# Kernel optimization log

Hardware: AMD Instinct MI355X
Metric: run time of the kernel (lower is better)

Reference implementation:

```python
import jax, jax.numpy as jnp
import numpy as np
import math

B, A, C = 16, 8732, 91
K = 400            # backend.topk_candidates (per-class top-k before NMS)
D = 200            # backend.detections_per_img
TOPK = 2           # extractor topk_candidates (classes returned per box)
SCORE_THRESH = 0.01
NMS_THRESH = 0.45
IMG = 300.0        # SSD300 image size (boxes clipped to [0, IMG])
BBOX_XFORM_CLIP = math.log(1000.0 / 16.0)


def setup_inputs() -> dict:
    key = jax.random.key(0)
    k1, k2, k3, k4 = jax.random.split(key, 4)
    cls_logits = jax.random.normal(k1, (B, A, C), jnp.float32)
    bbox_regression = jax.random.normal(k2, (B, A, 4), jnp.float32) * 0.5
    # valid anchors in xyxy with positive width/height
    cxcy = jax.random.uniform(k3, (A, 2), jnp.float32, 0.0, IMG)
    wh = jax.random.uniform(k4, (A, 2), jnp.float32, 8.0, 96.0)
    anchors = jnp.concatenate([cxcy - 0.5 * wh, cxcy + 0.5 * wh], axis=-1)
    return {"cls_logits": cls_logits, "bbox_regression": bbox_regression, "anchors": anchors}


def _decode(rel, anchors):
    # torchvision BoxCoder.decode_single, weights (10, 10, 5, 5)
    wa = anchors[:, 2] - anchors[:, 0]
    ha = anchors[:, 3] - anchors[:, 1]
    cxa = anchors[:, 0] + 0.5 * wa
    cya = anchors[:, 1] + 0.5 * ha
    dx = rel[:, 0] / 10.0
    dy = rel[:, 1] / 10.0
    dw = jnp.minimum(rel[:, 2] / 5.0, BBOX_XFORM_CLIP)
    dh = jnp.minimum(rel[:, 3] / 5.0, BBOX_XFORM_CLIP)
    cx = dx * wa + cxa
    cy = dy * ha + cya
    w = jnp.exp(dw) * wa
    h = jnp.exp(dh) * ha
    boxes = jnp.stack([cx - 0.5 * w, cy - 0.5 * h, cx + 0.5 * w, cy + 0.5 * h], axis=-1)
    return jnp.clip(boxes, 0.0, IMG)  # clip_boxes_to_image


def _iou_one_vs_all(box, boxes):
    x1 = jnp.maximum(box[0], boxes[:, 0])
    y1 = jnp.maximum(box[1], boxes[:, 1])
    x2 = jnp.minimum(box[2], boxes[:, 2])
    y2 = jnp.minimum(box[3], boxes[:, 3])
    inter = jnp.clip(x2 - x1, 0.0) * jnp.clip(y2 - y1, 0.0)
    a1 = (box[2] - box[0]) * (box[3] - box[1])
    a2 = (boxes[:, 2] - boxes[:, 0]) * (boxes[:, 3] - boxes[:, 1])
    return inter / (a1 + a2 - inter + 1e-9)


def _image_forward(logits, rel, anchors):
    probs = jax.nn.softmax(logits, axis=-1)          # [A, C]
    boxes = _decode(rel, anchors)                    # [A, 4]
    # per-class threshold + top-k (labels 1..C-1), padded fixed-size version
    fg = probs[:, 1:]                                # [A, C-1]
    masked = jnp.where(fg > SCORE_THRESH, fg, -1.0)
    vals, idxs = jax.lax.top_k(masked.T, K)          # [C-1, K]
    cand_boxes = boxes[idxs]                         # [C-1, K, 4]
    cand_all = probs[idxs]                           # [C-1, K, C]
    labels = jnp.broadcast_to(jnp.arange(1, C, dtype=jnp.int32)[:, None], (C - 1, K))
    valid = vals > SCORE_THRESH
    N = (C - 1) * K
    fb = cand_boxes.reshape(N, 4)
    fs = vals.reshape(N)
    fl = labels.reshape(N)
    fa = cand_all.reshape(N, C)
    fv = valid.reshape(N)
    # batched_nms: offset boxes per class so different classes never overlap
    off = fl.astype(jnp.float32) * (IMG + 2.0)
    ob = fb + off[:, None]
    s0 = jnp.where(fv, fs, -jnp.inf)

    def body(i, carry):
        s, keep, kscore = carry
        j = jnp.argmax(s)
        keep = keep.at[i].set(j.astype(jnp.int32))
        kscore = kscore.at[i].set(s[j])
        iou = _iou_one_vs_all(ob[j], ob)
        s = jnp.where(iou > NMS_THRESH, -jnp.inf, s)
        return s, keep, kscore

    _, keep, kscore = jax.lax.fori_loop(
        0, D, body,
        (s0, jnp.zeros(D, jnp.int32), jnp.full((D,), -jnp.inf, jnp.float32)))
    kvalid = kscore > -jnp.inf                       # padding rows (fewer than D dets)
    out_boxes = jnp.where(kvalid[:, None], fb[keep], 0.0)          # [D, 4]
    top_scores, tidx = jax.lax.top_k(fa[keep][:, 1:], TOPK)        # [D, TOPK]
    top_scores = jnp.where(kvalid[:, None], top_scores, 0.0)
    out_labels = jnp.where(kvalid[:, None], tidx + 1, 0)
    return out_boxes, top_scores, out_labels


def reference(cls_logits, bbox_regression, anchors):
    return jax.vmap(_image_forward, in_axes=(0, 0, None))(cls_logits, bbox_regression, anchors)
```

## Files before the change

### kernel.cpp

```cpp
#include <hip/hip_runtime.h>
#include <cstdint>
#include <cstddef>

#define B_N   16
#define A_N   8732
#define C_N   91
#define FG_N  90
#define K_TOP 400
#define D_N   200
#define NTASK (B_N * FG_N)
#define K1_APB 128
#define K1_NBLK ((A_N + K1_APB - 1) / K1_APB)
#define K4_T  1024
#define NBIN  2048

__global__ __launch_bounds__(128) void k1_softmax_decode(
    const float* __restrict__ cls, const float* __restrict__ reg,
    const float* __restrict__ anc, float* __restrict__ probs_t,
    float* __restrict__ boxes)
{
#pragma clang fp contract(off)
  __shared__ float4 lds4[(K1_APB * C_N + 3) / 4];
  float* lds = (float*)lds4;
  const int bb = blockIdx.x;
  const int b = bb / K1_NBLK;
  const int blk = bb - b * K1_NBLK;
  const int a0 = blk * K1_APB;
  const int nloc = (A_N - a0) < K1_APB ? (A_N - a0) : K1_APB;
  const int tid = threadIdx.x;

  const size_t gbase_f4 = ((size_t)(b * A_N + a0) * C_N) >> 2;
  const size_t TOT_F4 = ((size_t)B_N * A_N * C_N) >> 2;
  const float4* cls4 = (const float4*)cls;
  constexpr int NF4 = (K1_APB * C_N) / 4;
  for (int i = tid; i < NF4; i += K1_APB) {
    size_t g = gbase_f4 + i;
    if (g < TOT_F4) lds4[i] = cls4[g];
  }
  __syncthreads();

  if (tid >= nloc) return;
  const int a = a0 + tid;
  const int tg = b * A_N + a;
  float* lg = lds + tid * C_N;

  float m = lg[0];
  for (int c = 1; c < C_N; ++c) m = fmaxf(m, lg[c]);
  float s = 0.0f;
  for (int c = 0; c < C_N; ++c) {
    float e = expf(lg[c] - m);
    s += e;
    lg[c] = e;
  }
  for (int c = 1; c < C_N; ++c)
    probs_t[((size_t)b * FG_N + (c - 1)) * A_N + a] = lg[c] / s;

  float4 rl = *(const float4*)(reg + (size_t)tg * 4);
  float4 an = *(const float4*)(anc + (size_t)a * 4);
  float wa = an.z - an.x;
  float ha = an.w - an.y;
  float cxa = an.x + 0.5f * wa;
  float cya = an.y + 0.5f * ha;
  float dx = rl.x / 10.0f;
  float dy = rl.y / 10.0f;
  const float clipv = 4.135166556742356f;
  float dw = fminf(rl.z / 5.0f, clipv);
  float dh = fminf(rl.w / 5.0f, clipv);
  float t1 = dx * wa;  float cx = t1 + cxa;
  float t2 = dy * ha;  float cy = t2 + cya;
  float w = expf(dw) * wa;
  float h = expf(dh) * ha;
  float4 out;
  out.x = fminf(fmaxf(cx - 0.5f * w, 0.0f), 300.0f);
  out.y = fminf(fmaxf(cy - 0.5f * h, 0.0f), 300.0f);
  out.z = fminf(fmaxf(cx + 0.5f * w, 0.0f), 300.0f);
  out.w = fminf(fmaxf(cy + 0.5f * h, 0.0f), 300.0f);
  *(float4*)(boxes + (size_t)tg * 4) = out;
}

__device__ __forceinline__ void scan_select(int* hist, int nbins, int need,
                                            int tid, int* chunk, int* res)
{
  int per = nbins >> 8;
  if (tid < 256) {
    int s = 0;
    for (int i = 0; i < per; ++i) s += hist[tid * per + i];
    chunk[tid] = s;
  }
  __syncthreads();
  if (tid == 0) {
    int cum = 0;
    for (int t2 = 255; t2 >= 0; --t2) { int v = chunk[t2]; chunk[t2] = cum; cum += v; }
  }
  __syncthreads();
  if (tid < 256) {
    int cum = chunk[tid];
    for (int i = per - 1; i >= 0; --i) {
      int bn = tid * per + i;
      int h = hist[bn];
      if (cum < need && need <= cum + h) { res[0] = bn; res[1] = cum; }
      cum += h;
    }
  }
  __syncthreads();
}

__device__ __forceinline__ void desc_scan256(int* chunk, int* s_total, int tid)
{
  if (tid < 64) {
    const int l = tid;
    int e0 = chunk[4 * l + 0];
    int e1 = chunk[4 * l + 1];
    int e2 = chunk[4 * l + 2];
    int e3 = chunk[4 * l + 3];
    int ls = e0 + e1 + e2 + e3;
    int suf = ls;
#pragma unroll
    for (int d = 1; d < 64; d <<= 1) {
      int o = __shfl(suf, l + d, 64);
      if (l + d < 64) suf += o;
    }
    int excl = suf - ls;
    chunk[4 * l + 3] = excl;
    chunk[4 * l + 2] = excl + e3;
    chunk[4 * l + 1] = excl + e3 + e2;
    chunk[4 * l + 0] = excl + e3 + e2 + e1;
    if (l == 0) *s_total = suf;
  }
}

__global__ __launch_bounds__(256) void k23_topk_nms(
    const float* __restrict__ probs_t, const float* __restrict__ boxes,
    int* __restrict__ topk_anchor,
    unsigned long long* __restrict__ kept_key, int* __restrict__ kept_cnt)
{
#pragma clang fp contract(off)
  __shared__ __align__(16) int cnt[NBIN];
  __shared__ unsigned long long sorted[1024];
  __shared__ int chunk[256];
  __shared__ int res[2];
  __shared__ int s_total;
  __shared__ int s_bad;
  __shared__ int s_lcnt;
  __shared__ unsigned long long s_supm[4];
  __shared__ int s_nk;
  const int task = blockIdx.x;
  const int tid = threadIdx.x;
  const float* sc = probs_t + (size_t)task * A_N;
  const float4* sc4 = (const float4*)sc;
  constexpr int NV4 = A_N >> 2;

  for (int i = tid; i < NBIN; i += 256) cnt[i] = 0;
  if (tid == 0) s_bad = 0;
  __syncthreads();

  for (int i = tid; i < NV4; i += 256) {
    float4 p4 = sc4[i];
    if (p4.x > 0.01f) atomicAdd(&cnt[(__float_as_uint(p4.x) >> 15) & 0x7FFu], 1);
    if (p4.y > 0.01f) atomicAdd(&cnt[(__float_as_uint(p4.y) >> 15) & 0x7FFu], 1);
    if (p4.z > 0.01f) atomicAdd(&cnt[(__float_as_uint(p4.z) >> 15) & 0x7FFu], 1);
    if (p4.w > 0.01f) atomicAdd(&cnt[(__float_as_uint(p4.w) >> 15) & 0x7FFu], 1);
  }
  __syncthreads();
  {
    int s = 0;
    for (int i = 0; i < 8; ++i) s += cnt[tid * 8 + i];
    chunk[tid] = s;
  }
  __syncthreads();
  desc_scan256(chunk, &s_total, tid);
  __syncthreads();
  {
    int acc = chunk[tid];
    for (int i = 7; i >= 0; --i) {
      int bn = tid * 8 + i;
      int h = cnt[bn];
      cnt[bn] = acc;
      acc += h;
    }
  }
  __syncthreads();
  const int total = s_total;
  const int ksel = total < K_TOP ? total : K_TOP;

  for (int i = tid; i < NV4; i += 256) {
    float4 p4 = sc4[i];
    const unsigned a0 = (unsigned)(i * 4);
    if (p4.x > 0.01f) {
      unsigned k = __float_as_uint(p4.x);
      int pos = atomicAdd(&cnt[(k >> 15) & 0x7FFu], 1);
      if (pos < 1024)
        sorted[pos] = ((unsigned long long)k << 32) | (0xFFFFFFFFu - a0);
    }
    if (p4.y > 0.01f) {
      unsigned k = __float_as_uint(p4.y);
      int pos = atomicAdd(&cnt[(k >> 15) & 0x7FFu], 1);
      if (pos < 1024)
        sorted[pos] = ((unsigned long long)k << 32) | (0xFFFFFFFFu - (a0 + 1));
    }
    if (p4.z > 0.01f) {
      unsigned k = __float_as_uint(p4.z);
      int pos = atomicAdd(&cnt[(k >> 15) & 0x7FFu], 1);
      if (pos < 1024)
        sorted[pos] = ((unsigned long long)k << 32) | (0xFFFFFFFFu - (a0 + 2));
    }
    if (p4.w > 0.01f) {
      unsigned k = __float_as_uint(p4.w);
      int pos = atomicAdd(&cnt[(k >> 15) & 0x7FFu], 1);
      if (pos < 1024)
        sorted[pos] = ((unsigned long long)k << 32) | (0xFFFFFFFFu - (a0 + 3));
    }
  }
  __syncthreads();
  for (int i = 0; i < 8; ++i) {
    int bn = tid * 8 + i;
    int end0 = cnt[bn];
    int start = (bn < NBIN - 1) ? cnt[bn + 1] : 0;
    int cb = end0 - start;
    if (cb > 1 && start < K_TOP) {
      if (end0 > 1024) { s_bad = 1; continue; }
      for (int q = start + 1; q < end0; ++q) {
        unsigned long long v = sorted[q];
        int j = q - 1;
        while (j >= start && sorted[j] < v) { sorted[j + 1] = sorted[j]; --j; }
        sorted[j + 1] = v;
      }
    }
  }
  __syncthreads();

  if (s_bad) {
    for (int i = tid; i < NBIN; i += 256) cnt[i] = 0;
    __syncthreads();
    for (int a = tid; a < A_N; a += 256) {
      float p = sc[a];
      if (p > 0.01f) atomicAdd(&cnt[__float_as_uint(p) >> 21], 1);
    }
    __syncthreads();
    int need = K_TOP;
    scan_select(cnt, 2048, need, tid, chunk, res);
    const unsigned b1 = (unsigned)res[0];
    const int above1 = res[1];
    const int in1 = cnt[b1];
    __syncthreads();
    unsigned cutoff;
    if (above1 + in1 <= 1024) {
      cutoff = b1 << 21;
    } else {
      need -= above1;
      for (int i = tid; i < NBIN; i += 256) cnt[i] = 0;
      __syncthreads();
      for (int a = tid; a < A_N; a += 256) {
        float p = sc[a];
        if (p > 0.01f) {
          unsigned k = __float_as_uint(p);
          if ((k >> 21) == b1) atomicAdd(&cnt[(k >> 10) & 0x7FFu], 1);
        }
      }
      __syncthreads();
      scan_select(cnt, 2048, need, tid, chunk, res);
      const unsigned b2 = (unsigned)res[0];
      need -= res[1];
      const unsigned pre22 = (b1 << 11) | b2;
      __syncthreads();
      for (int i = tid; i < 1024; i += 256) cnt[i] = 0;
      __syncthreads();
      for (int a = tid; a < A_N; a += 256) {
        float p = sc[a];
        if (p > 0.01f) {
          unsigned k = __float_as_uint(p);
          if ((k >> 10) == pre22) atomicAdd(&cnt[k & 0x3FFu], 1);
        }
      }
      __syncthreads();
      scan_select(cnt, 1024, need, tid, chunk, res);
      cutoff = (pre22 << 10) | (unsigned)res[0];
      __syncthreads();
    }
    if (tid == 0) s_lcnt = 0;
    __syncthreads();
    for (int a = tid; a < A_N; a += 256) {
      float p = sc[a];
      if (p > 0.01f) {
        unsigned k = __float_as_uint(p);
        if (k >= cutoff) {
          int pos = atomicAdd(&s_lcnt, 1);
          if (pos < 1024)
            sorted[pos] = ((unsigned long long)k << 32) | (unsigned)(0xFFFFFFFFu - (unsigned)a);
        }
      }
    }
    __syncthreads();
    const int n = s_lcnt < 1024 ? s_lcnt : 1024;
    const int W = (n <= 512) ? 512 : 1024;
    for (int i = tid; i < W; i += 256) if (i >= n) sorted[i] = 0ULL;
    __syncthreads();
    for (int kk = 2; kk <= W; kk <<= 1) {
      for (int jj = kk >> 1; jj > 0; jj >>= 1) {
        for (int i = tid; i < W; i += 256) {
          int ix = i ^ jj;
          if (ix > i) {
            unsigned long long va = sorted[i], vb = sorted[ix];
            bool desc = ((i & kk) == 0);
            if (desc ? (va < vb) : (va > vb)) { sorted[i] = vb; sorted[ix] = va; }
          }
        }
        __syncthreads();
      }
    }
  }

  for (int r = tid; r < ksel; r += 256) {
    unsigned long long v = sorted[r];
    topk_anchor[(size_t)task * K_TOP + r] =
        (int)(0xFFFFFFFFu - (unsigned)(v & 0xFFFFFFFFull));
  }
  if (tid == 0) s_nk = 0;
  __syncthreads();

  float4* keptb  = (float4*)cnt;
  float*  kepta  = (float*)(cnt + 800);
  int*    keptr  = cnt + 1000;
  float4* chunkb = (float4*)(cnt + 1200);
  unsigned long long* colpart =
      (unsigned long long*)(cnt + 1456);

  const int wid  = tid >> 6;
  const int lane = tid & 63;
  const int b = task / FG_N;
  const int c = task - b * FG_N;
  const float off = (float)(c + 1) * 302.0f;
  const float* bx = boxes + (size_t)b * (A_N * 4);

  float4 nxt = make_float4(0.0f, 0.0f, 0.0f, 0.0f);
  if (lane < ksel) {
    int a0 = (int)(0xFFFFFFFFu - (unsigned)(sorted[lane] & 0xFFFFFFFFull));
    nxt = *(const float4*)(bx + (size_t)a0 * 4);
  }
  for (int c0 = 0; c0 < ksel; c0 += 64) {
    float4 cur = nxt;
    int nidx = c0 + 64 + lane;
    if (nidx < ksel) {
      int an = (int)(0xFFFFFFFFu - (unsigned)(sorted[nidx] & 0xFFFFFFFFull));
      nxt = *(const float4*)(bx + (size_t)an * 4);
    }
    const int rem = ksel - c0;
    cur.x += off; cur.y += off; cur.z += off; cur.w += off;
    const float area = (cur.z - cur.x) * (cur.w - cur.y);
    const int nk = s_nk;

    chunkb[lane] = cur;
    unsigned long long part = 0ULL;
    {
      const int jn = rem < 64 ? rem : 64;
      const int j0 = wid << 4;
      const int j1 = (j0 + 16) < jn ? (j0 + 16) : jn;
      for (int j = j0; j < j1; ++j) {
        float4 bj = chunkb[j];
        float ja = (bj.z - bj.x) * (bj.w - bj.y);
        float ix1 = fmaxf(bj.x, cur.x);
        float iy1 = fmaxf(bj.y, cur.y);
        float ix2 = fminf(bj.z, cur.z);
        float iy2 = fminf(bj.w, cur.w);
        float inter = fmaxf(ix2 - ix1, 0.0f) * fmaxf(iy2 - iy1, 0.0f);
        float denom = ja + area - inter + 1e-9f;
        float thr = 0.45f * denom;
        bool s_sup = inter > thr;
        bool amb = fabsf(inter - thr) <= 1.5e-6f * thr;
        if (amb) s_sup = (inter / denom) > 0.45f;
        if (s_sup && j != lane) part |= 1ULL << j;
      }
    }
    colpart[(wid << 6) | lane] = part;

    bool sup = false;
    for (int k = wid; k < nk; k += 4) {
      if (__all(sup)) break;
      float4 kb = keptb[k];
      float  ka = kepta[k];
      float ix1 = fmaxf(cur.x, kb.x);
      float iy1 = fmaxf(cur.y, kb.y);
      float ix2 = fminf(cur.z, kb.z);
      float iy2 = fminf(cur.w, kb.w);
      float inter = fmaxf(ix2 - ix1, 0.0f) * fmaxf(iy2 - iy1, 0.0f);
      float denom = ka + area - inter + 1e-9f;
      float thr = 0.45f * denom;
      bool s_sup = inter > thr;
      bool amb = fabsf(inter - thr) <= 1.5e-6f * thr;
      if (amb) s_sup = (inter / denom) > 0.45f;
      sup = sup || s_sup;
    }
    s_supm[wid] = __ballot(sup);
    __syncthreads();

    if (wid == 0) {
      unsigned long long col = colpart[lane] | colpart[64 | lane] |
                               colpart[128 | lane] | colpart[192 | lane];
      const unsigned long long vmask =
          (rem >= 64) ? ~0ULL : ((1ULL << rem) - 1ULL);
      unsigned long long todo =
          vmask & ~(s_supm[0] | s_supm[1] | s_supm[2] | s_supm[3]);
      unsigned long long surv = 0ULL;
      int ns = 0;
      const int room = D_N - nk;
      while (todo) {
        if (ns == room) break;
        int j = __ffsll((unsigned long long)todo) - 1;
        surv |= 1ULL << j;
        ++ns;
        todo &= ~(1ULL << j);
        bool msup = (col >> j) & 1ULL;
        unsigned long long supj = __ballot(msup);
        todo &= ~supj;
      }
      if ((surv >> lane) & 1ULL) {
        int my = nk + __popcll(surv & ((1ULL << lane) - 1ULL));
        keptb[my] = cur;
        kepta[my] = area;
        keptr[my] = c0 + lane;
      }
      if (lane == 0) s_nk = nk + ns;
    }
    __syncthreads();
    if (s_nk >= D_N) break;
  }

  const int nkf = s_nk;
  for (int k = tid; k < nkf; k += 256) {
    int r = keptr[k];
    unsigned sb = (unsigned)(sorted[r] >> 32);
    kept_key[(size_t)task * D_N + k] =
        ((unsigned long long)sb << 32) |
        (unsigned)(0xFFFFFFFFu - (unsigned)(c * K_TOP + r));
  }
  if (tid == 0) kept_cnt[task] = nkf;
}

__global__ __launch_bounds__(K4_T) void k4_sel(
    const unsigned long long* __restrict__ kept_key,
    const int* __restrict__ kept_cnt, int* __restrict__ pick_flat)
{
  __shared__ __align__(16) int hist[4096];
  __shared__ unsigned long long sorted[1024];
  __shared__ int chunk[256];
  __shared__ int res[2];
  __shared__ int s_total;
  __shared__ int s_bad;
  __shared__ int s_lcnt;
  __shared__ int s_cnts[FG_N];
  const int b = blockIdx.x;
  const int tid = threadIdx.x;
  const unsigned long long* kb = kept_key + (size_t)b * FG_N * D_N;

  if (tid < FG_N) s_cnts[tid] = kept_cnt[b * FG_N + tid];
  for (int i = tid; i < 4096; i += K4_T) hist[i] = 0;
  if (tid == 0) s_bad = 0;
  __syncthreads();

  for (int idx = tid; idx < FG_N * D_N; idx += K4_T) {
    int c = idx / D_N, r = idx - c * D_N;
    if (r < s_cnts[c])
      atomicAdd(&hist[(int)((kb[idx] >> 46) & 0xFFFull)], 1);
  }
  __syncthreads();
  if (tid < 256) {
    int s = 0;
    for (int i = 0; i < 16; ++i) s += hist[tid * 16 + i];
    chunk[tid] = s;
  }
  __syncthreads();
  desc_scan256(chunk, &s_total, tid);
  __syncthreads();
  if (tid < 256) {
    int acc = chunk[tid];
    for (int i = 15; i >= 0; --i) {
      int bn = tid * 16 + i;
      int h = hist[bn];
      hist[bn] = acc;
      acc += h;
    }
  }
  __syncthreads();
  const int total = s_total;
  const int npick = total < D_N ? total : D_N;

  for (int idx = tid; idx < FG_N * D_N; idx += K4_T) {
    int c = idx / D_N, r = idx - c * D_N;
    if (r < s_cnts[c]) {
      unsigned long long k = kb[idx];
      int pos = atomicAdd(&hist[(int)((k >> 46) & 0xFFFull)], 1);
      if (pos < 1024) sorted[pos] = k;
    }
  }
  __syncthreads();
  for (int i = 0; i < 4; ++i) {
    int bn = tid * 4 + i;
    int end0 = hist[bn];
    int start = (bn < 4095) ? hist[bn + 1] : 0;
    int cb = end0 - start;
    if (cb > 1 && start < D_N) {
      if (end0 > 1024) { s_bad = 1; continue; }
      for (int q = start + 1; q < end0; ++q) {
        unsigned long long v = sorted[q];
        int j = q - 1;
        while (j >= start && sorted[j] < v) { sorted[j + 1] = sorted[j]; --j; }
        sorted[j + 1] = v;
      }
    }
  }
  __syncthreads();

  if (s_bad) {
    for (int i = tid; i < 4096; i += K4_T) hist[i] = 0;
    if (tid == 0) s_lcnt = 0;
    __syncthreads();
    for (int idx = tid; idx < FG_N * D_N; idx += K4_T) {
      int c = idx / D_N, r = idx - c * D_N;
      if (r < s_cnts[c]) {
        unsigned long long k = kb[idx];
        atomicAdd(&hist[(int)(k >> 52)], 1);
      }
    }
    __syncthreads();
    unsigned cutoff32 = 1u;
    if (total > D_N) {
      int need = D_N;
      scan_select(hist, 4096, need, tid, chunk, res);
      const unsigned b1 = (unsigned)res[0];
      const int above1 = res[1];
      const int in1 = hist[b1];
      __syncthreads();
      if (above1 + in1 <= 1024) {
        cutoff32 = b1 << 20;
      } else {
        need -= above1;
        for (int i = tid; i < 4096; i += K4_T) hist[i] = 0;
        __syncthreads();
        for (int idx = tid; idx < FG_N * D_N; idx += K4_T) {
          int c = idx / D_N, r = idx - c * D_N;
          if (r < s_cnts[c]) {
            unsigned long long k = kb[idx];
            if ((unsigned)(k >> 52) == b1)
              atomicAdd(&hist[(int)((k >> 40) & 0xFFFull)], 1);
          }
        }
        __syncthreads();
        scan_select(hist, 4096, need, tid, chunk, res);
        const unsigned b2 = (unsigned)res[0];
        need -= res[1];
        const unsigned pre12 = (b1 << 12) | b2;
        __syncthreads();
        if (tid < 256) hist[tid] = 0;
        __syncthreads();
        for (int idx = tid; idx < FG_N * D_N; idx += K4_T) {
          int c = idx / D_N, r = idx - c * D_N;
          if (r < s_cnts[c]) {
            unsigned long long k = kb[idx];
            if ((unsigned)(k >> 40) == pre12)
              atomicAdd(&hist[(int)((k >> 32) & 0xFFull)], 1);
          }
        }
        __syncthreads();
        scan_select(hist, 256, need, tid, chunk, res);
        cutoff32 = (pre12 << 8) | (unsigned)res[0];
        __syncthreads();
      }
    }
    const unsigned long long cutkey = (unsigned long long)cutoff32 << 32;
    for (int idx = tid; idx < FG_N * D_N; idx += K4_T) {
      int c = idx / D_N, r = idx - c * D_N;
      if (r < s_cnts[c]) {
        unsigned long long k = kb[idx];
        if (k >= cutkey) {
          int pos = atomicAdd(&s_lcnt, 1);
          if (pos < 1024) sorted[pos] = k;
        }
      }
    }
    __syncthreads();
    const int n = s_lcnt < 1024 ? s_lcnt : 1024;
    const int W = (n <= 256) ? 256 : (n <= 512) ? 512 : 1024;
    for (int i = tid; i < W; i += K4_T) if (i >= n) sorted[i] = 0ULL;
    __syncthreads();
    for (int kk = 2; kk <= W; kk <<= 1) {
      for (int jj = kk >> 1; jj > 0; jj >>= 1) {
        for (int i = tid; i < W; i += K4_T) {
          int ix = i ^ jj;
          if (ix > i) {
            unsigned long long va = sorted[i], vb = sorted[ix];
            bool desc = ((i & kk) == 0);
            if (desc ? (va < vb) : (va > vb)) { sorted[i] = vb; sorted[ix] = va; }
          }
        }
        __syncthreads();
      }
    }
  }

  for (int i = tid; i < D_N; i += K4_T) {
    int v = -1;
    if (i < npick)
      v = (int)(0xFFFFFFFFu - (unsigned)(sorted[i] & 0xFFFFFFFFull));
    pick_flat[b * D_N + i] = v;
  }
}

__global__ __launch_bounds__(256) void k5_out(
    const float* __restrict__ probs_t, const float* __restrict__ boxes,
    const int* __restrict__ topk_anchor, const int* __restrict__ pick_flat,
    float* __restrict__ out)
{
  const int wid  = threadIdx.x >> 6;
  const int lane = threadIdx.x & 63;
  const int pick = blockIdx.x * 4 + wid;
  const int b = pick / D_N;
  float* ob = out + (size_t)pick * 4;
  float* os = out + (size_t)B_N * D_N * 4 + (size_t)pick * 2;
  float* ol = out + (size_t)B_N * D_N * 6 + (size_t)pick * 2;
  const int flat = pick_flat[pick];
  if (flat < 0) {
    if (lane == 0) {
      ob[0] = 0.0f; ob[1] = 0.0f; ob[2] = 0.0f; ob[3] = 0.0f;
      os[0] = 0.0f; os[1] = 0.0f;
      ol[0] = 0.0f; ol[1] = 0.0f;
    }
    return;
  }
  const int c = flat / K_TOP;
  const int r = flat - c * K_TOP;
  const int anchor = topk_anchor[((size_t)b * FG_N + c) * K_TOP + r];
  const float* pp = probs_t + (size_t)b * FG_N * A_N + anchor;

  unsigned long long hi, lo = 0ULL;
  {
    float p = pp[(size_t)lane * A_N];
    hi = ((unsigned long long)__float_as_uint(p) << 32) | (0xFFFFFFFFu - (unsigned)lane);
  }
  if (lane + 64 < FG_N) {
    float p = pp[(size_t)(lane + 64) * A_N];
    unsigned long long k2 = ((unsigned long long)__float_as_uint(p) << 32) |
                            (0xFFFFFFFFu - (unsigned)(lane + 64));
    if (k2 > hi) { lo = hi; hi = k2; } else lo = k2;
  }
#pragma unroll
  for (int d = 1; d < 64; d <<= 1) {
    unsigned long long oh = __shfl_xor(hi, d, 64);
    unsigned long long ol2 = __shfl_xor(lo, d, 64);
    unsigned long long nh = hi > oh ? hi : oh;
    unsigned long long mn = hi > oh ? oh : hi;
    unsigned long long ml = lo > ol2 ? lo : ol2;
    hi = nh;
    lo = mn > ml ? mn : ml;
  }
  if (lane == 0) {
    float4 bp = *(const float4*)(boxes + ((size_t)b * A_N + anchor) * 4);
    *(float4*)ob = bp;
    unsigned cc1 = 0xFFFFFFFFu - (unsigned)(hi & 0xFFFFFFFFull);
    unsigned cc2 = 0xFFFFFFFFu - (unsigned)(lo & 0xFFFFFFFFull);
    os[0] = __uint_as_float((unsigned)(hi >> 32));
    os[1] = __uint_as_float((unsigned)(lo >> 32));
    ol[0] = (float)(cc1 + 1);
    ol[1] = (float)(cc2 + 1);
  }
}

extern "C" void kernel_launch(void* const* d_in, const int* in_sizes, int n_in,
                              void* d_out, int out_size, void* d_ws, size_t ws_size,
                              hipStream_t stream)
{
  (void)in_sizes; (void)n_in; (void)out_size; (void)ws_size;
  const float* cls = (const float*)d_in[0];
  const float* reg = (const float*)d_in[1];
  const float* anc = (const float*)d_in[2];

  char* w = (char*)d_ws;
  size_t off = 0;
  auto carve = [&](size_t bytes) -> char* {
    char* p = w + off;
    off += (bytes + 255) & ~(size_t)255;
    return p;
  };
  float* probs_t                = (float*)carve((size_t)B_N * FG_N * A_N * 4);
  float* boxes                  = (float*)carve((size_t)B_N * A_N * 4 * 4);
  int* topk_anchor              = (int*)carve((size_t)NTASK * K_TOP * 4);
  unsigned long long* kept_key  = (unsigned long long*)carve((size_t)NTASK * D_N * 8);
  int* kept_cnt                 = (int*)carve((size_t)NTASK * 4);
  int* pick_flat                = (int*)carve((size_t)B_N * D_N * 4);

  hipLaunchKernelGGL(k1_softmax_decode, dim3(B_N * K1_NBLK), dim3(K1_APB), 0, stream,
                     cls, reg, anc, probs_t, boxes);
  hipLaunchKernelGGL(k23_topk_nms, dim3(NTASK), dim3(256), 0, stream,
                     probs_t, boxes, topk_anchor, kept_key, kept_cnt);
  hipLaunchKernelGGL(k4_sel, dim3(B_N), dim3(K4_T), 0, stream,
                     kept_key, kept_cnt, pick_flat);
  hipLaunchKernelGGL(k5_out, dim3(B_N * D_N / 4), dim3(256), 0, stream,
                     probs_t, boxes, topk_anchor, pick_flat, (float*)d_out);
}
```

Measured before the change: 258.7 us.

## Split softmax rows across 8 lanes with shuffle reductions; skip saturated-bin atomics

The softmax/decode kernel now assigns 8 threads per anchor, each loading up to 12 logits directly from global memory and combining max and sum with wave shuffles, instead of staging 128 rows in LDS and having one thread loop over 91 classes. This removes the LDS staging and serial per-thread loop and raises parallelism, but the global row loads are now strided and unaligned. The histogram scatter in the top-k/NMS kernel first reads the bin counter and skips the atomicAdd when the bin is already past capacity, and the NMS column-partial buffer is relocated into the sorted scratch region.

```diff
diff --git a/kernel.cpp b/kernel.cpp
--- a/kernel.cpp
+++ b/kernel.cpp
@@ -9,73 +9,73 @@
 #define K_TOP 400
 #define D_N   200
 #define NTASK (B_N * FG_N)
-#define K1_APB 128
-#define K1_NBLK ((A_N + K1_APB - 1) / K1_APB)
 #define K4_T  1024
 #define NBIN  2048
-
-__global__ __launch_bounds__(128) void k1_softmax_decode(
+#define K1B_T 256
+#define K1_ANB (K1B_T / 8)
+
+__global__ __launch_bounds__(K1B_T) void k1_softmax_decode(
     const float* __restrict__ cls, const float* __restrict__ reg,
     const float* __restrict__ anc, float* __restrict__ probs_t,
     float* __restrict__ boxes)
 {
 #pragma clang fp contract(off)
-  __shared__ float4 lds4[(K1_APB * C_N + 3) / 4];
-  float* lds = (float*)lds4;
-  const int bb = blockIdx.x;
-  const int b = bb / K1_NBLK;
-  const int blk = bb - b * K1_NBLK;
-  const int a0 = blk * K1_APB;
-  const int nloc = (A_N - a0) < K1_APB ? (A_N - a0) : K1_APB;
   const int tid = threadIdx.x;
-
-  const size_t gbase_f4 = ((size_t)(b * A_N + a0) * C_N) >> 2;
-  const size_t TOT_F4 = ((size_t)B_N * A_N * C_N) >> 2;
-  const float4* cls4 = (const float4*)cls;
-  constexpr int NF4 = (K1_APB * C_N) / 4;
-  for (int i = tid; i < NF4; i += K1_APB) {
-    size_t g = gbase_f4 + i;
-    if (g < TOT_F4) lds4[i] = cls4[g];
-  }
-  __syncthreads();
-
-  if (tid >= nloc) return;
-  const int a = a0 + tid;
-  const int tg = b * A_N + a;
-  float* lg = lds + tid * C_N;
-
-  float m = lg[0];
-  for (int c = 1; c < C_N; ++c) m = fmaxf(m, lg[c]);
+  const int g   = tid >> 3;
+  const int l8  = tid & 7;
+  const int gi  = blockIdx.x * K1_ANB + g;
+  const int b   = gi / A_N;
+  const int a   = gi - b * A_N;
+  const float* row = cls + (size_t)gi * C_N;
+  const int c0 = l8 * 12;
+  const int ne = (l8 == 7) ? 7 : 12;
+
+  float v[12];
+  for (int i = 0; i < ne; ++i) v[i] = row[c0 + i];
+
+  float m = v[0];
+  for (int i = 1; i < ne; ++i) m = fmaxf(m, v[i]);
+#pragma unroll
+  for (int d = 1; d < 8; d <<= 1) m = fmaxf(m, __shfl_xor(m, d, 64));
+
+  float e[12];
   float s = 0.0f;
-  for (int c = 0; c < C_N; ++c) {
-    float e = expf(lg[c] - m);
-    s += e;
-    lg[c] = e;
-  }
-  for (int c = 1; c < C_N; ++c)
-    probs_t[((size_t)b * FG_N + (c - 1)) * A_N + a] = lg[c] / s;
-
-  float4 rl = *(const float4*)(reg + (size_t)tg * 4);
-  float4 an = *(const float4*)(anc + (size_t)a * 4);
-  float wa = an.z - an.x;
-  float ha = an.w - an.y;
-  float cxa = an.x + 0.5f * wa;
-  float cya = an.y + 0.5f * ha;
-  float dx = rl.x / 10.0f;
-  float dy = rl.y / 10.0f;
-  const float clipv = 4.135166556742356f;
-  float dw = fminf(rl.z / 5.0f, clipv);
-  float dh = fminf(rl.w / 5.0f, clipv);
-  float t1 = dx * wa;  float cx = t1 + cxa;
-  float t2 = dy * ha;  float cy = t2 + cya;
-  float w = expf(dw) * wa;
-  float h = expf(dh) * ha;
-  float4 out;
-  out.x = fminf(fmaxf(cx - 0.5f * w, 0.0f), 300.0f);
-  out.y = fminf(fmaxf(cy - 0.5f * h, 0.0f), 300.0f);
-  out.z = fminf(fmaxf(cx + 0.5f * w, 0.0f), 300.0f);
-  out.w = fminf(fmaxf(cy + 0.5f * h, 0.0f), 300.0f);
-  *(float4*)(boxes + (size_t)tg * 4) = out;
+  for (int i = 0; i < ne; ++i) {
+    e[i] = expf(v[i] - m);
+    s += e[i];
+  }
+#pragma unroll
+  for (int d = 1; d < 8; d <<= 1) s += __shfl_xor(s, d, 64);
+
+  for (int i = 0; i < ne; ++i) {
+    int c = c0 + i;
+    if (c >= 1)
+      probs_t[((size_t)b * FG_N + (c - 1)) * A_N + a] = e[i] / s;
+  }
+
+  if (l8 == 7) {
+    float4 rl = *(const float4*)(reg + (size_t)gi * 4);
+    float4 an = *(const float4*)(anc + (size_t)a * 4);
+    float wa = an.z - an.x;
+    float ha = an.w - an.y;
+    float cxa = an.x + 0.5f * wa;
+    float cya = an.y + 0.5f * ha;
+    float dx = rl.x / 10.0f;
+    float dy = rl.y / 10.0f;
+    const float clipv = 4.135166556742356f;
+    float dw = fminf(rl.z / 5.0f, clipv);
+    float dh = fminf(rl.w / 5.0f, clipv);
+    float t1 = dx * wa;  float cx = t1 + cxa;
+    float t2 = dy * ha;  float cy = t2 + cya;
+    float w = expf(dw) * wa;
+    float h = expf(dh) * ha;
+    float4 out;
+    out.x = fminf(fmaxf(cx - 0.5f * w, 0.0f), 300.0f);
+    out.y = fminf(fmaxf(cy - 0.5f * h, 0.0f), 300.0f);
+    out.z = fminf(fmaxf(cx + 0.5f * w, 0.0f), 300.0f);
+    out.w = fminf(fmaxf(cy + 0.5f * h, 0.0f), 300.0f);
+    *(float4*)(boxes + (size_t)gi * 4) = out;
+  }
 }
 
 __device__ __forceinline__ void scan_select(int* hist, int nbins, int need,
@@ -188,27 +188,39 @@
     const unsigned a0 = (unsigned)(i * 4);
     if (p4.x > 0.01f) {
       unsigned k = __float_as_uint(p4.x);
-      int pos = atomicAdd(&cnt[(k >> 15) & 0x7FFu], 1);
-      if (pos < 1024)
-        sorted[pos] = ((unsigned long long)k << 32) | (0xFFFFFFFFu - a0);
+      int bin = (int)((k >> 15) & 0x7FFu);
+      if (cnt[bin] <= 1024) {
+        int pos = atomicAdd(&cnt[bin], 1);
+        if (pos < 1024)
+          sorted[pos] = ((unsigned long long)k << 32) | (0xFFFFFFFFu - a0);
+      }
     }
     if (p4.y > 0.01f) {
       unsigned k = __float_as_uint(p4.y);
-      int pos = atomicAdd(&cnt[(k >> 15) & 0x7FFu], 1);
-      if (pos < 1024)
-        sorted[pos] = ((unsigned long long)k << 32) | (0xFFFFFFFFu - (a0 + 1));
+      int bin = (int)((k >> 15) & 0x7FFu);
+      if (cnt[bin] <= 1024) {
+        int pos = atomicAdd(&cnt[bin], 1);
+        if (pos < 1024)
+          sorted[pos] = ((unsigned long long)k << 32) | (0xFFFFFFFFu - (a0 + 1));
+      }
     }
     if (p4.z > 0.01f) {
       unsigned k = __float_as_uint(p4.z);
-      int pos = atomicAdd(&cnt[(k >> 15) & 0x7FFu], 1);
-      if (pos < 1024)
-        sorted[pos] = ((unsigned long long)k << 32) | (0xFFFFFFFFu - (a0 + 2));
+      int bin = (int)((k >> 15) & 0x7FFu);
+      if (cnt[bin] <= 1024) {
+        int pos = atomicAdd(&cnt[bin], 1);
+        if (pos < 1024)
+          sorted[pos] = ((unsigned long long)k << 32) | (0xFFFFFFFFu - (a0 + 2));
+      }
     }
     if (p4.w > 0.01f) {
       unsigned k = __float_as_uint(p4.w);
-      int pos = atomicAdd(&cnt[(k >> 15) & 0x7FFu], 1);
-      if (pos < 1024)
-        sorted[pos] = ((unsigned long long)k << 32) | (0xFFFFFFFFu - (a0 + 3));
+      int bin = (int)((k >> 15) & 0x7FFu);
+      if (cnt[bin] <= 1024) {
+        int pos = atomicAdd(&cnt[bin], 1);
+        if (pos < 1024)
+          sorted[pos] = ((unsigned long long)k << 32) | (0xFFFFFFFFu - (a0 + 3));
+      }
     }
   }
   __syncthreads();
@@ -322,8 +334,7 @@
   float*  kepta  = (float*)(cnt + 800);
   int*    keptr  = cnt + 1000;
   float4* chunkb = (float4*)(cnt + 1200);
-  unsigned long long* colpart =
-      (unsigned long long*)(cnt + 1456);
+  unsigned long long* colpart = &sorted[640];
 
   const int wid  = tid >> 6;
   const int lane = tid & 63;
@@ -354,7 +365,7 @@
     {
       const int jn = rem < 64 ? rem : 64;
       const int j0 = wid << 4;
-      const int j1 = (j0 + 16) < jn ? (j0 + 16) : jn;
+      int j1 = j0 + 16; if (j1 > jn) j1 = jn;
       for (int j = j0; j < j1; ++j) {
         float4 bj = chunkb[j];
         float ja = (bj.z - bj.x) * (bj.w - bj.y);
@@ -687,7 +698,7 @@
   int* kept_cnt                 = (int*)carve((size_t)NTASK * 4);
   int* pick_flat                = (int*)carve((size_t)B_N * D_N * 4);
 
-  hipLaunchKernelGGL(k1_softmax_decode, dim3(B_N * K1_NBLK), dim3(K1_APB), 0, stream,
+  hipLaunchKernelGGL(k1_softmax_decode, dim3((B_N * A_N) / K1_ANB), dim3(K1B_T), 0, stream,
                      cls, reg, anc, probs_t, boxes);
   hipLaunchKernelGGL(k23_topk_nms, dim3(NTASK), dim3(256), 0, stream,
                      probs_t, boxes, topk_anchor, kept_key, kept_cnt);
```

Result: faster. 251.0 us (-3.0%).
